# Optimization experiments

Hardware: AMD Instinct MI355X
Metric: run time of the kernel (lower is better)

The kernel has to match this reference:

```python
import jax, jax.numpy as jnp
import numpy as np

EMBD_DIM = 1024
NUM_HEADS = 16
HEAD_DIM = EMBD_DIM // NUM_HEADS


def setup_inputs() -> dict:
    key = jax.random.key(0)
    ks = jax.random.split(key, 9)
    B, S, D = 2, 2048, EMBD_DIM
    scale = 1.0 / np.sqrt(D)
    return {
        "x": jax.random.normal(ks[0], (B, S, D), dtype=jnp.float32),
        "wq": jax.random.normal(ks[1], (D, D), dtype=jnp.float32) * scale,
        "bq": jnp.zeros((D,), dtype=jnp.float32),
        "wk": jax.random.normal(ks[2], (D, D), dtype=jnp.float32) * scale,
        "bk": jnp.zeros((D,), dtype=jnp.float32),
        "wv": jax.random.normal(ks[3], (D, D), dtype=jnp.float32) * scale,
        "bv": jnp.zeros((D,), dtype=jnp.float32),
        "wo": jax.random.normal(ks[4], (D, D), dtype=jnp.float32) * scale,
        "bo": jnp.zeros((D,), dtype=jnp.float32),
    }


def reference(x, wq, bq, wk, bk, wv, bv, wo, bo):
    B, S, D = x.shape
    H, hd = NUM_HEADS, HEAD_DIM
    # projections: weights stored as (in, out) so y = x @ w + b
    q = (x @ wq + bq).reshape(B, S, H, hd).transpose(0, 2, 1, 3)  # [B,H,S,hd]
    k = (x @ wk + bk).reshape(B, S, H, hd).transpose(0, 2, 1, 3)
    v = (x @ wv + bv).reshape(B, S, H, hd).transpose(0, 2, 1, 3)
    scores = jnp.einsum("bhqd,bhkd->bhqk", q, k) / jnp.sqrt(jnp.float32(hd))
    causal = jnp.tril(jnp.ones((S, S), dtype=bool))  # [S,S]
    neg = jnp.finfo(scores.dtype).min
    scores = jnp.where(causal[None, None, :, :], scores, neg)
    attn = jax.nn.softmax(scores, axis=-1)
    out = jnp.einsum("bhqk,bhkd->bhqd", attn, v)  # [B,H,S,hd]
    out = out.transpose(0, 2, 1, 3).reshape(B, S, D)
    return out @ wo + bo
```

## Files before the change

kernel.cpp:

```cpp
#include <hip/hip_runtime.h>
#include <math.h>

#define S_LEN 2048
#define BATCH 2
#define DMODEL 1024
#define NHEADS 16
#define MROWS 4096

typedef short bf8 __attribute__((ext_vector_type(8)));
typedef float f32x4 __attribute__((ext_vector_type(4)));
typedef unsigned short u16;

static __device__ inline u16 f2bf(float f) {
    union { float f; unsigned u; } v; v.f = f;
    unsigned r = v.u + 0x7fffu + ((v.u >> 16) & 1u);
    return (u16)(r >> 16);
}

static __device__ inline void load16(const void* g, void* l) {
    __builtin_amdgcn_global_load_lds(
        (const __attribute__((address_space(1))) unsigned int*)g,
        (__attribute__((address_space(3))) unsigned int*)l, 16, 0, 0);
}

__global__ __launch_bounds__(256) void prep_kernel(
    const float* __restrict__ x, u16* __restrict__ xb,
    const float* __restrict__ W0, const float* __restrict__ W1,
    const float* __restrict__ W2, const float* __restrict__ W3,
    u16* __restrict__ wT) {
    const int bx = blockIdx.x, t = threadIdx.x;
    if (bx < 2048) {
        int i = bx * 256 + t;
        const float4* p = (const float4*)x + (size_t)i * 2;
        float4 a = p[0], b = p[1];
        u16 tmp[8] = {f2bf(a.x), f2bf(a.y), f2bf(a.z), f2bf(a.w),
                      f2bf(b.x), f2bf(b.y), f2bf(b.z), f2bf(b.w)};
        ((uint4*)xb)[i] = *(uint4*)tmp;
        return;
    }
    __shared__ u16 Ls[64][65];
    const int id = bx - 2048;
    const int z = id >> 8, rem = id & 255;
    const int n0 = (rem & 15) * 64, k0 = (rem >> 4) * 64;
    const float* W = z == 0 ? W0 : z == 1 ? W1 : z == 2 ? W2 : W3;
    u16* Wt = wT + (size_t)z * 1024 * 1024;
    const int r = t >> 2, c4 = (t & 3) * 16;
    const float* p = W + (size_t)(k0 + r) * 1024 + n0 + c4;
#pragma unroll
    for (int i = 0; i < 16; i += 4) {
        float4 v = *(const float4*)(p + i);
        Ls[r][c4 + i + 0] = f2bf(v.x);
        Ls[r][c4 + i + 1] = f2bf(v.y);
        Ls[r][c4 + i + 2] = f2bf(v.z);
        Ls[r][c4 + i + 3] = f2bf(v.w);
    }
    __syncthreads();
    u16 tmp[16];
#pragma unroll
    for (int i = 0; i < 16; i++) tmp[i] = Ls[c4 + i][r];
    uint4* q = (uint4*)(Wt + (size_t)(n0 + r) * 1024 + k0 + c4);
    q[0] = *(uint4*)tmp;
    q[1] = *(uint4*)(tmp + 8);
}

template <int MODE>
__global__ __launch_bounds__(256) void gemm_mfma(
    const u16* __restrict__ A, const u16* __restrict__ Bt,
    const float* __restrict__ bqp, const float* __restrict__ bkp,
    const float* __restrict__ bvp,
    u16* __restrict__ qout, u16* __restrict__ kout, u16* __restrict__ vtout,
    float* __restrict__ fout, float qscale) {
    __shared__ __align__(16) u16 As[128 * 32];
    __shared__ __align__(16) u16 Bs[128 * 32];

    const int t = threadIdx.x, lane = t & 63, w = t >> 6;
    const int quad = lane >> 4, l16 = lane & 15;
    const int row0 = blockIdx.y * 128, col0 = blockIdx.x * 128;
    const int wr = (w >> 1) * 64, wc = (w & 1) * 64;
    const int K = DMODEL;

    const int srow = w * 32 + (lane >> 2);
    const int koff = (((lane & 3) ^ ((lane >> 3) & 3))) * 8;
    const u16* ag = A + (size_t)(row0 + srow) * K + koff;
    const u16* bg = Bt + (size_t)(col0 + srow) * K + koff;
    u16* lA0 = As + (w * 32) * 32;
    u16* lA1 = As + (w * 32 + 16) * 32;
    u16* lB0 = Bs + (w * 32) * 32;
    u16* lB1 = Bs + (w * 32 + 16) * 32;
    const size_t r16 = (size_t)16 * K;

    const int swz = (l16 >> 1) & 3;

    f32x4 acc[4][4] = {};

    for (int k0 = 0; k0 < K; k0 += 32) {
        load16(ag + k0, lA0);
        load16(ag + r16 + k0, lA1);
        load16(bg + k0, lB0);
        load16(bg + r16 + k0, lB1);
        __syncthreads();
        bf8 af[4], bfr[4];
#pragma unroll
        for (int mi = 0; mi < 4; mi++)
            af[mi] = *(const bf8*)&As[(wr + mi * 16 + l16) * 32 + (quad ^ swz) * 8];
#pragma unroll
        for (int ni = 0; ni < 4; ni++)
            bfr[ni] = *(const bf8*)&Bs[(wc + ni * 16 + l16) * 32 + (quad ^ swz) * 8];
#pragma unroll
        for (int mi = 0; mi < 4; mi++)
#pragma unroll
            for (int ni = 0; ni < 4; ni++)
                acc[mi][ni] = __builtin_amdgcn_mfma_f32_16x16x32_bf16(
                    af[mi], bfr[ni], acc[mi][ni], 0, 0, 0);
        __syncthreads();
    }

    const int sect = (col0 + wc) >> 10;
#pragma unroll
    for (int mi = 0; mi < 4; mi++) {
        const int r = row0 + wr + mi * 16 + quad * 4;
#pragma unroll
        for (int ni = 0; ni < 4; ni++) {
            const int c = col0 + wc + ni * 16 + l16;
            if (MODE == 1) {
                float bvv = bqp[c];
#pragma unroll
                for (int reg = 0; reg < 4; reg++)
                    fout[(size_t)(r + reg) * 1024 + c] = acc[mi][ni][reg] + bvv;
            } else {
                const int cl = c & 1023;
                const float* bp = sect == 0 ? bqp : sect == 1 ? bkp : bvp;
                float bvv = bp[cl];
                if (sect == 0) {
#pragma unroll
                    for (int reg = 0; reg < 4; reg++)
                        qout[(size_t)(r + reg) * 1024 + cl] =
                            f2bf((acc[mi][ni][reg] + bvv) * qscale);
                } else if (sect == 1) {
#pragma unroll
                    for (int reg = 0; reg < 4; reg++)
                        kout[(size_t)(r + reg) * 1024 + cl] =
                            f2bf(acc[mi][ni][reg] + bvv);
                } else {
                    u16 t4[4];
#pragma unroll
                    for (int reg = 0; reg < 4; reg++)
                        t4[reg] = f2bf(acc[mi][ni][reg] + bvv);
                    *(uint2*)(vtout + ((size_t)(r >> 11) * 1024 + cl) * S_LEN +
                              (r & 2047)) = *(uint2*)t4;
                }
            }
        }
    }
}

__global__ __launch_bounds__(256) void attn_kernel(const u16* __restrict__ Qg,
                                                   const u16* __restrict__ Kg,
                                                   const u16* __restrict__ Vt,
                                                   u16* __restrict__ Og) {
    __shared__ __align__(16) u16 Ks[2][64][32];
    __shared__ __align__(16) u16 Vs[2][64][32];
    __shared__ __align__(16) u16 Ps[4][16][64];

    const int t = threadIdx.x, lane = t & 63, w = t >> 6;
    const int quad = lane >> 4, l16 = lane & 15;
    const int pi = blockIdx.x;
    const int bh = blockIdx.y, b = bh >> 4, h = bh & 15;
    const size_t base = (size_t)b * S_LEN * DMODEL + h * 64;
    const size_t vbase = ((size_t)b * 1024 + h * 64) * S_LEN;
    const int sr = t >> 2, sc = (t & 3) * 16;
    const int pl = sc >> 5;
    const int g0 = (sc >> 3) & 3;
    const int ss = (sr >> 1) & 3;
    const int swz = (l16 >> 1) & 3;
    const int pswz = l16 & 7;

    const u16* kp = Kg + base + (size_t)sr * DMODEL + sc;
    const u16* vp = Vt + vbase + (size_t)sr * S_LEN + sc;
    uint4 k0r = *(const uint4*)kp, k1r = *(const uint4*)(kp + 8);
    uint4 v0r = *(const uint4*)vp, v1r = *(const uint4*)(vp + 8);

#pragma unroll
    for (int seg = 0; seg < 2; seg++) {
        const int qt = seg == 0 ? pi : 31 - pi;
        const int niter = qt + 1;
        const int q0 = qt * 64;

        bf8 aq[2];
#pragma unroll
        for (int c = 0; c < 2; c++)
            aq[c] = *(const bf8*)(Qg + base +
                (size_t)(q0 + w * 16 + l16) * DMODEL + c * 32 + quad * 8);

        float lsum[4] = {};
        f32x4 o_acc[4] = {};

        for (int kt = 0; kt < niter; kt++) {
            __syncthreads();
            *(uint4*)&Ks[pl][sr][(g0 ^ ss) * 8] = k0r;
            *(uint4*)&Ks[pl][sr][((g0 + 1) ^ ss) * 8] = k1r;
            *(uint4*)&Vs[pl][sr][(g0 ^ ss) * 8] = v0r;
            *(uint4*)&Vs[pl][sr][((g0 + 1) ^ ss) * 8] = v1r;
            __syncthreads();
            if (!(seg == 1 && kt + 1 == niter)) {
                int nt = (kt + 1 < niter) ? kt + 1 : 0;
                size_t ok = (size_t)nt * 64 * DMODEL;
                int ov = nt * 64;
                k0r = *(const uint4*)(kp + ok); k1r = *(const uint4*)(kp + ok + 8);
                v0r = *(const uint4*)(vp + ov); v1r = *(const uint4*)(vp + ov + 8);
            }

            f32x4 scv[4] = {};
#pragma unroll
            for (int c = 0; c < 2; c++)
#pragma unroll
                for (int ns = 0; ns < 4; ns++) {
                    bf8 bk = *(const bf8*)&Ks[c][ns * 16 + l16][(quad ^ swz) * 8];
                    scv[ns] = __builtin_amdgcn_mfma_f32_16x16x32_bf16(
                        aq[c], bk, scv[ns], 0, 0, 0);
                }

            const bool diag = (kt == qt);
            const int myq = w * 16 + quad * 4;
#pragma unroll
            for (int ns = 0; ns < 4; ns++) {
                int key = ns * 16 + l16;
#pragma unroll
                for (int r = 0; r < 4; r++) {
                    float p = (diag && key > myq + r)
                                  ? 0.f
                                  : __builtin_amdgcn_exp2f(scv[ns][r]);
                    lsum[r] += p;
                    const int q = quad * 4 + r;
                    const int g = ns * 2 + (l16 >> 3);
                    Ps[w][q][((g ^ (q & 7)) * 8) + (l16 & 7)] =
                        (u16)(__float_as_uint(p) >> 16);
                }
            }
            asm volatile("s_waitcnt lgkmcnt(0)" ::: "memory");

#pragma unroll
            for (int kc = 0; kc < 2; kc++) {
                bf8 apv = *(const bf8*)&Ps[w][l16][((kc * 4 + quad) ^ pswz) * 8];
#pragma unroll
                for (int ds = 0; ds < 4; ds++) {
                    bf8 bvv = *(const bf8*)&Vs[kc][ds * 16 + l16][(quad ^ swz) * 8];
                    o_acc[ds] = __builtin_amdgcn_mfma_f32_16x16x32_bf16(
                        apv, bvv, o_acc[ds], 0, 0, 0);
                }
            }
        }

#pragma unroll
        for (int r = 0; r < 4; r++) {
            float l = lsum[r];
#pragma unroll
            for (int off = 8; off >= 1; off >>= 1) l += __shfl_xor(l, off, 64);
            float inv = 1.f / l;
            int qq = q0 + w * 16 + quad * 4 + r;
#pragma unroll
            for (int ds = 0; ds < 4; ds++)
                Og[base + (size_t)qq * DMODEL + ds * 16 + l16] =
                    f2bf(o_acc[ds][r] * inv);
        }
    }
}

extern "C" void kernel_launch(void* const* d_in, const int* in_sizes, int n_in,
                              void* d_out, int out_size, void* d_ws, size_t ws_size,
                              hipStream_t stream) {
    const float* x  = (const float*)d_in[0];
    const float* wq = (const float*)d_in[1];
    const float* bq = (const float*)d_in[2];
    const float* wk = (const float*)d_in[3];
    const float* bk = (const float*)d_in[4];
    const float* wv = (const float*)d_in[5];
    const float* bv = (const float*)d_in[6];
    const float* wo = (const float*)d_in[7];
    const float* bo = (const float*)d_in[8];
    float* out = (float*)d_out;

    const size_t E = (size_t)MROWS * DMODEL;
    u16* xb  = (u16*)d_out;
    u16* vt  = xb + E;
    u16* wT  = (u16*)d_ws;
    u16* woT = wT + 3145728;
    u16* qb  = wT + 4194304;
    u16* kb  = qb + E;
    u16* ob  = kb + E;

    dim3 blk(256);
    prep_kernel<<<3072, blk, 0, stream>>>(x, xb, wq, wk, wv, wo, wT);

    gemm_mfma<0><<<dim3(24, 32), blk, 0, stream>>>(
        xb, wT, bq, bk, bv, qb, kb, vt, nullptr, 0.18033688011112042f);

    dim3 agrid(16, BATCH * NHEADS);
    attn_kernel<<<agrid, blk, 0, stream>>>(qb, kb, vt, ob);

    gemm_mfma<1><<<dim3(8, 32), blk, 0, stream>>>(
        ob, woT, bo, nullptr, nullptr, nullptr, nullptr, nullptr, out, 1.0f);
}
```

Measured before the change: 207.3 us.

## Double attention key tile to 128 and retile output GEMM to 64-row blocks

The attention kernel now stages two 64-key tiles per iteration (128 keys), halving the number of sync/stage iterations and issuing 16 QK MFMAs per pass. On the odd-tile diagonal the extra keys are masked, which adds some wasted compute. The GEMM swaps operand roles so each thread's accumulator holds four consecutive features, enabling vectorized float4/uint2 stores and per-row bias loads. The output projection uses 64-row tiles, doubling its grid to 512 blocks for better CU occupancy, but V-transpose stores become scalar.

```diff
diff --git a/kernel.cpp b/kernel.cpp
--- a/kernel.cpp
+++ b/kernel.cpp
@@ -70,20 +70,24 @@
     const float* __restrict__ bvp,
     u16* __restrict__ qout, u16* __restrict__ kout, u16* __restrict__ vtout,
     float* __restrict__ fout, float qscale) {
-    __shared__ __align__(16) u16 As[128 * 32];
+    constexpr int TM = (MODE == 1) ? 64 : 128;
+    constexpr int MI = (MODE == 1) ? 2 : 4;
+    __shared__ __align__(16) u16 As[TM * 32];
     __shared__ __align__(16) u16 Bs[128 * 32];
 
     const int t = threadIdx.x, lane = t & 63, w = t >> 6;
     const int quad = lane >> 4, l16 = lane & 15;
-    const int row0 = blockIdx.y * 128, col0 = blockIdx.x * 128;
-    const int wr = (w >> 1) * 64, wc = (w & 1) * 64;
+    const int row0 = blockIdx.y * TM, col0 = blockIdx.x * 128;
+    const int fq = (MODE == 1) ? w * 32 : (w & 1) * 64;
+    const int xq = (MODE == 1) ? 0 : (w >> 1) * 64;
     const int K = DMODEL;
 
-    const int srow = w * 32 + (lane >> 2);
     const int koff = (((lane & 3) ^ ((lane >> 3) & 3))) * 8;
-    const u16* ag = A + (size_t)(row0 + srow) * K + koff;
-    const u16* bg = Bt + (size_t)(col0 + srow) * K + koff;
-    u16* lA0 = As + (w * 32) * 32;
+    const int srowA = (MODE == 1) ? (w * 16 + (lane >> 2)) : (w * 32 + (lane >> 2));
+    const int srowB = w * 32 + (lane >> 2);
+    const u16* ag = A + (size_t)(row0 + srowA) * K + koff;
+    const u16* bg = Bt + (size_t)(col0 + srowB) * K + koff;
+    u16* lA0 = As + ((MODE == 1) ? (w * 16) : (w * 32)) * 32;
     u16* lA1 = As + (w * 32 + 16) * 32;
     u16* lB0 = Bs + (w * 32) * 32;
     u16* lB1 = Bs + (w * 32 + 16) * 32;
@@ -91,63 +95,68 @@
 
     const int swz = (l16 >> 1) & 3;
 
-    f32x4 acc[4][4] = {};
+    f32x4 acc[MI][4] = {};
 
     for (int k0 = 0; k0 < K; k0 += 32) {
         load16(ag + k0, lA0);
-        load16(ag + r16 + k0, lA1);
+        if (MODE == 0) load16(ag + r16 + k0, lA1);
         load16(bg + k0, lB0);
         load16(bg + r16 + k0, lB1);
         __syncthreads();
-        bf8 af[4], bfr[4];
-#pragma unroll
-        for (int mi = 0; mi < 4; mi++)
-            af[mi] = *(const bf8*)&As[(wr + mi * 16 + l16) * 32 + (quad ^ swz) * 8];
+        bf8 xf[4], wf[MI];
 #pragma unroll
         for (int ni = 0; ni < 4; ni++)
-            bfr[ni] = *(const bf8*)&Bs[(wc + ni * 16 + l16) * 32 + (quad ^ swz) * 8];
-#pragma unroll
-        for (int mi = 0; mi < 4; mi++)
+            xf[ni] = *(const bf8*)&As[(xq + ni * 16 + l16) * 32 + (quad ^ swz) * 8];
+#pragma unroll
+        for (int mi = 0; mi < MI; mi++)
+            wf[mi] = *(const bf8*)&Bs[(fq + mi * 16 + l16) * 32 + (quad ^ swz) * 8];
+#pragma unroll
+        for (int mi = 0; mi < MI; mi++)
 #pragma unroll
             for (int ni = 0; ni < 4; ni++)
                 acc[mi][ni] = __builtin_amdgcn_mfma_f32_16x16x32_bf16(
-                    af[mi], bfr[ni], acc[mi][ni], 0, 0, 0);
+                    wf[mi], xf[ni], acc[mi][ni], 0, 0, 0);
         __syncthreads();
     }
 
-    const int sect = (col0 + wc) >> 10;
-#pragma unroll
-    for (int mi = 0; mi < 4; mi++) {
-        const int r = row0 + wr + mi * 16 + quad * 4;
+    const int sect = (col0 + fq) >> 10;
+#pragma unroll
+    for (int mi = 0; mi < MI; mi++) {
+        const int featb = col0 + fq + mi * 16 + quad * 4;
+        float b4[4];
+#pragma unroll
+        for (int reg = 0; reg < 4; reg++)
+            b4[reg] = (MODE == 1 ? bqp : (sect == 0 ? bqp : sect == 1 ? bkp : bvp))
+                          [(featb + reg) & 1023];
 #pragma unroll
         for (int ni = 0; ni < 4; ni++) {
-            const int c = col0 + wc + ni * 16 + l16;
+            const int xrow = row0 + xq + ni * 16 + l16;
             if (MODE == 1) {
-                float bvv = bqp[c];
-#pragma unroll
-                for (int reg = 0; reg < 4; reg++)
-                    fout[(size_t)(r + reg) * 1024 + c] = acc[mi][ni][reg] + bvv;
+                float4 o;
+                o.x = acc[mi][ni][0] + b4[0];
+                o.y = acc[mi][ni][1] + b4[1];
+                o.z = acc[mi][ni][2] + b4[2];
+                o.w = acc[mi][ni][3] + b4[3];
+                *(float4*)(fout + (size_t)xrow * 1024 + featb) = o;
             } else {
-                const int cl = c & 1023;
-                const float* bp = sect == 0 ? bqp : sect == 1 ? bkp : bvp;
-                float bvv = bp[cl];
+                const int cf = featb & 1023;
                 if (sect == 0) {
+                    u16 t4[4];
 #pragma unroll
                     for (int reg = 0; reg < 4; reg++)
-                        qout[(size_t)(r + reg) * 1024 + cl] =
-                            f2bf((acc[mi][ni][reg] + bvv) * qscale);
+                        t4[reg] = f2bf((acc[mi][ni][reg] + b4[reg]) * qscale);
+                    *(uint2*)(qout + (size_t)xrow * 1024 + cf) = *(uint2*)t4;
                 } else if (sect == 1) {
+                    u16 t4[4];
 #pragma unroll
                     for (int reg = 0; reg < 4; reg++)
-                        kout[(size_t)(r + reg) * 1024 + cl] =
-                            f2bf(acc[mi][ni][reg] + bvv);
+                        t4[reg] = f2bf(acc[mi][ni][reg] + b4[reg]);
+                    *(uint2*)(kout + (size_t)xrow * 1024 + cf) = *(uint2*)t4;
                 } else {
-                    u16 t4[4];
 #pragma unroll
                     for (int reg = 0; reg < 4; reg++)
-                        t4[reg] = f2bf(acc[mi][ni][reg] + bvv);
-                    *(uint2*)(vtout + ((size_t)(r >> 11) * 1024 + cl) * S_LEN +
-                              (r & 2047)) = *(uint2*)t4;
+                        vtout[((size_t)(xrow >> 11) * 1024 + cf + reg) * S_LEN +
+                              (xrow & 2047)] = f2bf(acc[mi][ni][reg] + b4[reg]);
                 }
             }
         }
@@ -158,9 +167,9 @@
                                                    const u16* __restrict__ Kg,
                                                    const u16* __restrict__ Vt,
                                                    u16* __restrict__ Og) {
-    __shared__ __align__(16) u16 Ks[2][64][32];
-    __shared__ __align__(16) u16 Vs[2][64][32];
-    __shared__ __align__(16) u16 Ps[4][16][64];
+    __shared__ __align__(16) u16 Ks[2][128][32];
+    __shared__ __align__(16) u16 Vs[4][64][32];
+    __shared__ __align__(16) u16 Ps[4][16][128];
 
     const int t = threadIdx.x, lane = t & 63, w = t >> 6;
     const int quad = lane >> 4, l16 = lane & 15;
@@ -173,17 +182,21 @@
     const int g0 = (sc >> 3) & 3;
     const int ss = (sr >> 1) & 3;
     const int swz = (l16 >> 1) & 3;
-    const int pswz = l16 & 7;
 
     const u16* kp = Kg + base + (size_t)sr * DMODEL + sc;
     const u16* vp = Vt + vbase + (size_t)sr * S_LEN + sc;
+    const size_t kr64 = (size_t)64 * DMODEL;
+
     uint4 k0r = *(const uint4*)kp, k1r = *(const uint4*)(kp + 8);
+    uint4 k2r = *(const uint4*)(kp + kr64), k3r = *(const uint4*)(kp + kr64 + 8);
     uint4 v0r = *(const uint4*)vp, v1r = *(const uint4*)(vp + 8);
+    uint4 v2r = *(const uint4*)(vp + 64), v3r = *(const uint4*)(vp + 72);
 
 #pragma unroll
     for (int seg = 0; seg < 2; seg++) {
         const int qt = seg == 0 ? pi : 31 - pi;
         const int niter = qt + 1;
+        const int nd = (niter + 1) >> 1;
         const int q0 = qt * 64;
 
         bf8 aq[2];
@@ -195,56 +208,66 @@
         float lsum[4] = {};
         f32x4 o_acc[4] = {};
 
-        for (int kt = 0; kt < niter; kt++) {
+        for (int j = 0; j < nd; j++) {
             __syncthreads();
             *(uint4*)&Ks[pl][sr][(g0 ^ ss) * 8] = k0r;
             *(uint4*)&Ks[pl][sr][((g0 + 1) ^ ss) * 8] = k1r;
+            *(uint4*)&Ks[pl][sr + 64][(g0 ^ ss) * 8] = k2r;
+            *(uint4*)&Ks[pl][sr + 64][((g0 + 1) ^ ss) * 8] = k3r;
             *(uint4*)&Vs[pl][sr][(g0 ^ ss) * 8] = v0r;
             *(uint4*)&Vs[pl][sr][((g0 + 1) ^ ss) * 8] = v1r;
+            *(uint4*)&Vs[2 + pl][sr][(g0 ^ ss) * 8] = v2r;
+            *(uint4*)&Vs[2 + pl][sr][((g0 + 1) ^ ss) * 8] = v3r;
             __syncthreads();
-            if (!(seg == 1 && kt + 1 == niter)) {
-                int nt = (kt + 1 < niter) ? kt + 1 : 0;
-                size_t ok = (size_t)nt * 64 * DMODEL;
-                int ov = nt * 64;
-                k0r = *(const uint4*)(kp + ok); k1r = *(const uint4*)(kp + ok + 8);
-                v0r = *(const uint4*)(vp + ov); v1r = *(const uint4*)(vp + ov + 8);
+
+            if (j + 1 < nd || seg == 0) {
+                size_t ok = (j + 1 < nd) ? (size_t)(j + 1) * 128 * DMODEL : 0;
+                int ov = (j + 1 < nd) ? (j + 1) * 128 : 0;
+                k0r = *(const uint4*)(kp + ok);
+                k1r = *(const uint4*)(kp + ok + 8);
+                k2r = *(const uint4*)(kp + ok + kr64);
+                k3r = *(const uint4*)(kp + ok + kr64 + 8);
+                v0r = *(const uint4*)(vp + ov);
+                v1r = *(const uint4*)(vp + ov + 8);
+                v2r = *(const uint4*)(vp + ov + 64);
+                v3r = *(const uint4*)(vp + ov + 72);
             }
 
-            f32x4 scv[4] = {};
+            f32x4 scv[8] = {};
 #pragma unroll
             for (int c = 0; c < 2; c++)
 #pragma unroll
-                for (int ns = 0; ns < 4; ns++) {
+                for (int ns = 0; ns < 8; ns++) {
                     bf8 bk = *(const bf8*)&Ks[c][ns * 16 + l16][(quad ^ swz) * 8];
                     scv[ns] = __builtin_amdgcn_mfma_f32_16x16x32_bf16(
                         aq[c], bk, scv[ns], 0, 0, 0);
                 }
 
-            const bool diag = (kt == qt);
-            const int myq = w * 16 + quad * 4;
-#pragma unroll
-            for (int ns = 0; ns < 4; ns++) {
-                int key = ns * 16 + l16;
+            const bool lastd = (j == nd - 1);
+            const int qbase = q0 + w * 16 + quad * 4;
+#pragma unroll
+            for (int ns = 0; ns < 8; ns++) {
+                const int key_g = j * 128 + ns * 16 + l16;
+                const int g = ns * 2 + (l16 >> 3);
 #pragma unroll
                 for (int r = 0; r < 4; r++) {
-                    float p = (diag && key > myq + r)
+                    float p = (lastd && key_g > qbase + r)
                                   ? 0.f
                                   : __builtin_amdgcn_exp2f(scv[ns][r]);
                     lsum[r] += p;
                     const int q = quad * 4 + r;
-                    const int g = ns * 2 + (l16 >> 3);
-                    Ps[w][q][((g ^ (q & 7)) * 8) + (l16 & 7)] =
+                    Ps[w][q][(g ^ (q & 7)) * 8 + (l16 & 7)] =
                         (u16)(__float_as_uint(p) >> 16);
                 }
             }
             asm volatile("s_waitcnt lgkmcnt(0)" ::: "memory");
 
 #pragma unroll
-            for (int kc = 0; kc < 2; kc++) {
-                bf8 apv = *(const bf8*)&Ps[w][l16][((kc * 4 + quad) ^ pswz) * 8];
+            for (int kk = 0; kk < 4; kk++) {
+                bf8 apv = *(const bf8*)&Ps[w][l16][((kk * 4 + quad) ^ (l16 & 7)) * 8];
 #pragma unroll
                 for (int ds = 0; ds < 4; ds++) {
-                    bf8 bvv = *(const bf8*)&Vs[kc][ds * 16 + l16][(quad ^ swz) * 8];
+                    bf8 bvv = *(const bf8*)&Vs[kk][ds * 16 + l16][(quad ^ swz) * 8];
                     o_acc[ds] = __builtin_amdgcn_mfma_f32_16x16x32_bf16(
                         apv, bvv, o_acc[ds], 0, 0, 0);
                 }
@@ -298,6 +321,6 @@
     dim3 agrid(16, BATCH * NHEADS);
     attn_kernel<<<agrid, blk, 0, stream>>>(qb, kb, vt, ob);
 
-    gemm_mfma<1><<<dim3(8, 32), blk, 0, stream>>>(
+    gemm_mfma<1><<<dim3(8, 64), blk, 0, stream>>>(
         ob, woT, bo, nullptr, nullptr, nullptr, nullptr, nullptr, out, 1.0f);
 }
```

Result: no change. 207.0 us (-0.1%).
